# Optimization experiments

Measured on AMD Instinct MI355X. Metric: run time of the kernel, lower is better.

The kernel has to match this reference:

```python
import jax, jax.numpy as jnp
import numpy as np
from jax import lax

POOL_SIZE = 7
MERGE_INTERVAL = 1
NUM_FRAMES = 16_777_216  # 2**24, indices exact in float32
MAX_BEATS = NUM_FRAMES // 8  # fixed upper bound on number of merged-peak sections


def setup_inputs() -> dict:
    key = jax.random.key(0)
    logit = jax.random.normal(key, (1, NUM_FRAMES), dtype=jnp.float32)
    return {"logit": logit}


def reference(logit):
    # logit: (1, N)
    x = logit[0]  # (N,)
    N = x.shape[0]
    pad = POOL_SIZE // 2
    # max_pool1d, stride 1, same padding
    pooled = lax.reduce_window(x, -jnp.inf, lax.max,
                               window_dimensions=(POOL_SIZE,),
                               window_strides=(1,),
                               padding=((pad, pad),))
    # peak: position is a local max within the window AND value > 0
    peak = (x == pooled) & (x > 0)  # (N,) bool

    idx = jnp.arange(N, dtype=jnp.int32)
    # position of the most recent peak at or before each index (-1 if none)
    last_peak = lax.cummax(jnp.where(peak, idx, jnp.int32(-1)))
    # previous peak strictly before each index
    prev_peak = jnp.concatenate([jnp.full((1,), -1, jnp.int32), last_peak[:-1]])
    gap = idx - prev_peak
    # a peak starts a new section if gap to previous peak > merge_interval (first peak always new)
    is_new = peak & ((gap > MERGE_INTERVAL) | (prev_peak < 0))
    # section id per position (valid only at peaks); sections are contiguous 0..S-1
    section = jnp.cumsum(is_new.astype(jnp.int32)) - 1
    # route non-peaks to an overflow bucket
    seg_ids = jnp.where(peak, section, jnp.int32(MAX_BEATS))

    peak_f = peak.astype(jnp.float32)
    sum_peaks = jax.ops.segment_sum(idx.astype(jnp.float32) * peak_f, seg_ids,
                                    num_segments=MAX_BEATS + 1,
                                    indices_are_sorted=True)[:MAX_BEATS]
    count_peaks = jax.ops.segment_sum(peak_f, seg_ids,
                                      num_segments=MAX_BEATS + 1,
                                      indices_are_sorted=True)[:MAX_BEATS]
    # averaged beat positions; unused sections padded with -1 (torch returns a
    # dynamically-sized (1, num_sections) tensor; here first num_sections entries match)
    beats = jnp.where(count_peaks > 0,
                      sum_peaks / jnp.maximum(count_peaks, 1.0),
                      jnp.float32(-1.0))
    return beats[None, :]  # (1, MAX_BEATS)
```

## Files before the change

kernel.cpp:

```cpp
#include <hip/hip_runtime.h>
#include <cstdint>
#include <math.h>

#define N_FRAMES 16777216
#define MAX_BEATS (N_FRAMES / 8)
#define CHUNK 4096
#define NTHREADS 256
#define NBLOCKS (N_FRAMES / CHUNK)
#define TOTAL_MASKS ((size_t)NBLOCKS * 64)

typedef unsigned long long u64;
typedef unsigned int u32;

__device__ __forceinline__ bool peak_at_global(const float* __restrict__ x, int j) {
  if (j < 0 || j >= N_FRAMES) return false;
  const float c = x[j];
  if (!(c > 0.0f)) return false;
  float m = -INFINITY;
#pragma unroll
  for (int d = -3; d <= 3; ++d) {
    if (d == 0) continue;
    const int k = j + d;
    if (k >= 0 && k < N_FRAMES) m = fmaxf(m, x[k]);
  }
  return c >= m;
}

__global__ __launch_bounds__(NTHREADS) void k_count(const float* __restrict__ x,
                                                    int* __restrict__ blockCounts,
                                                    u64* __restrict__ masks) {
  __shared__ u32 m16[NTHREADS];
  __shared__ u32 s_pm1;
  const int b = blockIdx.x;
  const int g0 = b * CHUNK;
  const int t = threadIdx.x;
  const int gbase = g0 + t * 16;

  float v[24];
  if (gbase - 4 >= 0 && gbase + 20 <= N_FRAMES) {
    const float4* p = reinterpret_cast<const float4*>(x + gbase - 4);
#pragma unroll
    for (int k = 0; k < 6; ++k) {
      const float4 f = p[k];
      v[4 * k + 0] = f.x; v[4 * k + 1] = f.y; v[4 * k + 2] = f.z; v[4 * k + 3] = f.w;
    }
  } else {
#pragma unroll
    for (int k = 0; k < 24; ++k) {
      const int gi = gbase - 4 + k;
      v[k] = (gi >= 0 && gi < N_FRAMES) ? x[gi] : -INFINITY;
    }
  }

  u32 pm = 0;
#pragma unroll
  for (int e = 0; e < 16; ++e) {
    const float c = v[e + 4];
    float m = fmaxf(fmaxf(v[e + 1], v[e + 2]), fmaxf(v[e + 3], v[e + 5]));
    m = fmaxf(m, fmaxf(v[e + 6], v[e + 7]));
    pm |= (c > 0.0f && c >= m) ? (1u << e) : 0u;
  }
  m16[t] = pm;
  if (t == 0) {
    const float c = v[3];
    float m = fmaxf(fmaxf(v[0], v[1]), fmaxf(v[2], v[4]));
    m = fmaxf(m, fmaxf(v[5], v[6]));
    s_pm1 = (c > 0.0f && c >= m) ? 1u : 0u;
  }
  __syncthreads();

  if (t < 64) {
    const u64 m = (u64)m16[4 * t] | ((u64)m16[4 * t + 1] << 16) |
                  ((u64)m16[4 * t + 2] << 32) | ((u64)m16[4 * t + 3] << 48);
    masks[((size_t)b << 6) + t] = m;
    const u64 carry = (t == 0) ? (u64)s_pm1 : (u64)((m16[4 * t - 1] >> 15) & 1u);
    int cnt = __popcll(m & ~((m << 1) | carry));
#pragma unroll
    for (int off = 32; off; off >>= 1) cnt += __shfl_down(cnt, off, 64);
    if (t == 0) blockCounts[b] = cnt;
  }
}

__global__ __launch_bounds__(NTHREADS) void k_scan(const int* __restrict__ counts,
                                                   int* __restrict__ offsets) {
  __shared__ int wtot[4];
  const int t = threadIdx.x;
  const int w = t >> 6, lane = t & 63;
  int local[16];
  int s = 0;
#pragma unroll
  for (int e = 0; e < 16; ++e) { local[e] = counts[t * 16 + e]; s += local[e]; }
  int incl = s;
#pragma unroll
  for (int off = 1; off < 64; off <<= 1) {
    const int vv = __shfl_up(incl, off, 64);
    if (lane >= off) incl += vv;
  }
  if (lane == 63) wtot[w] = incl;
  __syncthreads();
  int wadd = 0;
  for (int ww = 0; ww < w; ++ww) wadd += wtot[ww];
  int excl = wadd + incl - s;
#pragma unroll
  for (int e = 0; e < 16; ++e) { offsets[t * 16 + e] = excl; excl += local[e]; }
  if (t == NTHREADS - 1) offsets[NBLOCKS] = excl;
}

__global__ __launch_bounds__(NTHREADS) void k_emit(const u64* __restrict__ masks,
                                                   const int* __restrict__ offsets,
                                                   float* __restrict__ out) {
  const int w = threadIdx.x >> 6, lane = threadIdx.x & 63;
  const int b = blockIdx.x * 4 + w;
  const size_t mi = ((size_t)b << 6) + lane;
  const u64 m = masks[mi];
  const u32 myb63 = (u32)(m >> 63);
  u32 prevb = __shfl_up(myb63, 1, 64);
  if (lane == 0) prevb = (b == 0) ? 0u : (u32)(masks[mi - 1] >> 63);
  u64 sm = m & ~((m << 1) | (u64)prevb);
  const int cnt = __popcll(sm);

  int incl = cnt;
#pragma unroll
  for (int off = 1; off < 64; off <<= 1) {
    const int vv = __shfl_up(incl, off, 64);
    if (lane >= off) incl += vv;
  }
  int sid = offsets[b] + incl - cnt;

  const int gbase = b * CHUNK + lane * 64;
  while (sm) {
    const int s = __builtin_ctzll(sm);
    sm &= sm - 1;
    const int i0 = gbase + s;
    const u64 above = m >> s;
    const int len = (~above == 0ull) ? (64 - s) : __builtin_ctzll(~above);
    int end = i0 + len - 1;
    if (s + len == 64) {
      size_t idx = mi + 1;
      while (idx < TOTAL_MASKS) {
        const u64 mm = masks[idx];
        if (~mm == 0ull) { end += 64; ++idx; }
        else { end += __builtin_ctzll(~mm); break; }
      }
    }
    if (sid < MAX_BEATS)
      out[sid] = (float)(((double)i0 + (double)end) * 0.5);
    ++sid;
  }

  const int total = offsets[NBLOCKS];
  const int lo = blockIdx.x * (MAX_BEATS / (NBLOCKS / 4));
  const int hi = lo + (MAX_BEATS / (NBLOCKS / 4));
  for (int i = max(lo, total) + (int)threadIdx.x; i < hi; i += NTHREADS)
    out[i] = -1.0f;
}

extern "C" void kernel_launch(void* const* d_in, const int* in_sizes, int n_in,
                              void* d_out, int out_size, void* d_ws, size_t ws_size,
                              hipStream_t stream) {
  const float* x = (const float*)d_in[0];
  float* out = (float*)d_out;

  u64* masks = (u64*)d_ws;
  int* counts = (int*)(masks + TOTAL_MASKS);
  int* offsets = counts + NBLOCKS;

  k_count<<<NBLOCKS, NTHREADS, 0, stream>>>(x, counts, masks);
  k_scan<<<1, NTHREADS, 0, stream>>>(counts, offsets);
  k_emit<<<NBLOCKS / 4, NTHREADS, 0, stream>>>(masks, offsets, out);
}
```

Measured before the change: 30.41 us.

## Drop the separate scan kernel and fold the offset scan into the emit kernel

Removes the single-block scan launch. Each emit block now reduces all 8192 per-wave counts itself and derives its own prefix offsets. The count kernel moves to 32 elements per thread with wave-level halos exchanged through shuffles instead of shared memory and block syncs, plus separable 3-wide max partials. Masks become 32-bit words. This saves one launch and its serialization, at the cost of every emit block redundantly reading 32 KB of counts.

```diff
diff --git a/kernel.cpp b/kernel.cpp
--- a/kernel.cpp
+++ b/kernel.cpp
@@ -4,143 +4,144 @@
 
 #define N_FRAMES 16777216
 #define MAX_BEATS (N_FRAMES / 8)
-#define CHUNK 4096
 #define NTHREADS 256
-#define NBLOCKS (N_FRAMES / CHUNK)
-#define TOTAL_MASKS ((size_t)NBLOCKS * 64)
+#define EPT 32
+#define EPB (NTHREADS * EPT)
+#define NBLOCKS (N_FRAMES / EPB)
+#define WCHUNK 2048
+#define NWCHUNK (N_FRAMES / WCHUNK)
+#define NMASK32 (N_FRAMES / 32)
 
-typedef unsigned long long u64;
 typedef unsigned int u32;
 
-__device__ __forceinline__ bool peak_at_global(const float* __restrict__ x, int j) {
-  if (j < 0 || j >= N_FRAMES) return false;
-  const float c = x[j];
-  if (!(c > 0.0f)) return false;
-  float m = -INFINITY;
+__global__ __launch_bounds__(NTHREADS) void k_count(const float* __restrict__ x,
+                                                    int* __restrict__ counts,
+                                                    u32* __restrict__ masks) {
+  const int t = threadIdx.x;
+  const int lane = t & 63;
+  const int wv = t >> 6;
+  const int q = blockIdx.x * 4 + wv;
+  const int gbase = q * WCHUNK + lane * EPT;
+
+  float v[40];
+  const float4* p = reinterpret_cast<const float4*>(x + gbase);
 #pragma unroll
-  for (int d = -3; d <= 3; ++d) {
-    if (d == 0) continue;
-    const int k = j + d;
-    if (k >= 0 && k < N_FRAMES) m = fmaxf(m, x[k]);
+  for (int k = 0; k < 8; ++k) {
+    const float4 f = p[k];
+    v[4 + 4 * k] = f.x; v[5 + 4 * k] = f.y; v[6 + 4 * k] = f.z; v[7 + 4 * k] = f.w;
   }
-  return c >= m;
-}
-
-__global__ __launch_bounds__(NTHREADS) void k_count(const float* __restrict__ x,
-                                                    int* __restrict__ blockCounts,
-                                                    u64* __restrict__ masks) {
-  __shared__ u32 m16[NTHREADS];
-  __shared__ u32 s_pm1;
-  const int b = blockIdx.x;
-  const int g0 = b * CHUNK;
-  const int t = threadIdx.x;
-  const int gbase = g0 + t * 16;
-
-  float v[24];
-  if (gbase - 4 >= 0 && gbase + 20 <= N_FRAMES) {
-    const float4* p = reinterpret_cast<const float4*>(x + gbase - 4);
 #pragma unroll
-    for (int k = 0; k < 6; ++k) {
-      const float4 f = p[k];
-      v[4 * k + 0] = f.x; v[4 * k + 1] = f.y; v[4 * k + 2] = f.z; v[4 * k + 3] = f.w;
+  for (int j = 0; j < 4; ++j) v[j] = __shfl_up(v[32 + j], 1, 64);
+#pragma unroll
+  for (int j = 0; j < 4; ++j) v[36 + j] = __shfl_down(v[4 + j], 1, 64);
+  if (lane == 0) {
+    if (gbase >= 4) {
+      const float4 f = *reinterpret_cast<const float4*>(x + gbase - 4);
+      v[0] = f.x; v[1] = f.y; v[2] = f.z; v[3] = f.w;
+    } else {
+      v[0] = v[1] = v[2] = v[3] = -INFINITY;
     }
-  } else {
-#pragma unroll
-    for (int k = 0; k < 24; ++k) {
-      const int gi = gbase - 4 + k;
-      v[k] = (gi >= 0 && gi < N_FRAMES) ? x[gi] : -INFINITY;
+  }
+  if (lane == 63) {
+    if (gbase + 36 <= N_FRAMES) {
+      const float4 f = *reinterpret_cast<const float4*>(x + gbase + 32);
+      v[36] = f.x; v[37] = f.y; v[38] = f.z; v[39] = f.w;
+    } else {
+      v[36] = v[37] = v[38] = v[39] = -INFINITY;
     }
   }
 
+  float Lt[37];
+#pragma unroll
+  for (int i = 0; i < 37; ++i) Lt[i] = fmaxf(fmaxf(v[i], v[i + 1]), v[i + 2]);
+
   u32 pm = 0;
 #pragma unroll
-  for (int e = 0; e < 16; ++e) {
+  for (int e = 0; e < 32; ++e) {
     const float c = v[e + 4];
-    float m = fmaxf(fmaxf(v[e + 1], v[e + 2]), fmaxf(v[e + 3], v[e + 5]));
-    m = fmaxf(m, fmaxf(v[e + 6], v[e + 7]));
-    pm |= (c > 0.0f && c >= m) ? (1u << e) : 0u;
+    const float m = fmaxf(Lt[e + 1], Lt[e + 5]);
+    if (c > 0.0f && c >= m) pm |= (1u << e);
   }
-  m16[t] = pm;
-  if (t == 0) {
+  masks[q * 64 + lane] = pm;
+
+  u32 prevbit = __shfl_up(pm, 1, 64) >> 31;
+  if (lane == 0) {
     const float c = v[3];
-    float m = fmaxf(fmaxf(v[0], v[1]), fmaxf(v[2], v[4]));
-    m = fmaxf(m, fmaxf(v[5], v[6]));
-    s_pm1 = (c > 0.0f && c >= m) ? 1u : 0u;
+    const float m = fmaxf(Lt[0], Lt[4]);
+    prevbit = (c > 0.0f && c >= m) ? 1u : 0u;
   }
-  __syncthreads();
-
-  if (t < 64) {
-    const u64 m = (u64)m16[4 * t] | ((u64)m16[4 * t + 1] << 16) |
-                  ((u64)m16[4 * t + 2] << 32) | ((u64)m16[4 * t + 3] << 48);
-    masks[((size_t)b << 6) + t] = m;
-    const u64 carry = (t == 0) ? (u64)s_pm1 : (u64)((m16[4 * t - 1] >> 15) & 1u);
-    int cnt = __popcll(m & ~((m << 1) | carry));
+  const u32 sm = pm & ~((pm << 1) | prevbit);
+  int cnt = __popc(sm);
 #pragma unroll
-    for (int off = 32; off; off >>= 1) cnt += __shfl_down(cnt, off, 64);
-    if (t == 0) blockCounts[b] = cnt;
-  }
+  for (int off = 32; off; off >>= 1) cnt += __shfl_down(cnt, off, 64);
+  if (lane == 0) counts[q] = cnt;
 }
 
-__global__ __launch_bounds__(NTHREADS) void k_scan(const int* __restrict__ counts,
-                                                   int* __restrict__ offsets) {
-  __shared__ int wtot[4];
+__global__ __launch_bounds__(NTHREADS) void k_emit(const u32* __restrict__ masks,
+                                                   const int* __restrict__ counts,
+                                                   float* __restrict__ out) {
+  __shared__ int s_wtot[4];
+  __shared__ int s_excl0[NTHREADS];
+  __shared__ int s_off[4];
+  __shared__ int s_total;
   const int t = threadIdx.x;
-  const int w = t >> 6, lane = t & 63;
-  int local[16];
+  const int lane = t & 63;
+  const int wv = t >> 6;
+
   int s = 0;
 #pragma unroll
-  for (int e = 0; e < 16; ++e) { local[e] = counts[t * 16 + e]; s += local[e]; }
+  for (int e = 0; e < 32; ++e) s += counts[t * 32 + e];
   int incl = s;
 #pragma unroll
   for (int off = 1; off < 64; off <<= 1) {
     const int vv = __shfl_up(incl, off, 64);
     if (lane >= off) incl += vv;
   }
-  if (lane == 63) wtot[w] = incl;
+  s_excl0[t] = incl - s;
+  if (lane == 63) s_wtot[wv] = incl;
   __syncthreads();
-  int wadd = 0;
-  for (int ww = 0; ww < w; ++ww) wadd += wtot[ww];
-  int excl = wadd + incl - s;
-#pragma unroll
-  for (int e = 0; e < 16; ++e) { offsets[t * 16 + e] = excl; excl += local[e]; }
-  if (t == NTHREADS - 1) offsets[NBLOCKS] = excl;
-}
+  if (t == 0) s_total = s_wtot[0] + s_wtot[1] + s_wtot[2] + s_wtot[3];
+  const int base = blockIdx.x * 4;
+  if (t < 4) {
+    const int target = base + t;
+    const int j = target >> 5, r = target & 31;
+    int wb = 0;
+    for (int ww = 0; ww < (j >> 6); ++ww) wb += s_wtot[ww];
+    int pfx = wb + s_excl0[j];
+    for (int e = 0; e < r; ++e) pfx += counts[j * 32 + e];
+    s_off[t] = pfx;
+  }
+  __syncthreads();
 
-__global__ __launch_bounds__(NTHREADS) void k_emit(const u64* __restrict__ masks,
-                                                   const int* __restrict__ offsets,
-                                                   float* __restrict__ out) {
-  const int w = threadIdx.x >> 6, lane = threadIdx.x & 63;
-  const int b = blockIdx.x * 4 + w;
-  const size_t mi = ((size_t)b << 6) + lane;
-  const u64 m = masks[mi];
-  const u32 myb63 = (u32)(m >> 63);
-  u32 prevb = __shfl_up(myb63, 1, 64);
-  if (lane == 0) prevb = (b == 0) ? 0u : (u32)(masks[mi - 1] >> 63);
-  u64 sm = m & ~((m << 1) | (u64)prevb);
-  const int cnt = __popcll(sm);
+  const int q = base + wv;
+  const u32 m = masks[q * 64 + lane];
+  u32 prevbit = __shfl_up(m, 1, 64) >> 31;
+  if (lane == 0) prevbit = (q == 0) ? 0u : (masks[q * 64 - 1] >> 31);
+  u32 sm = m & ~((m << 1) | prevbit);
+  const int cnt = __popc(sm);
 
-  int incl = cnt;
+  int incl2 = cnt;
 #pragma unroll
   for (int off = 1; off < 64; off <<= 1) {
-    const int vv = __shfl_up(incl, off, 64);
-    if (lane >= off) incl += vv;
+    const int vv = __shfl_up(incl2, off, 64);
+    if (lane >= off) incl2 += vv;
   }
-  int sid = offsets[b] + incl - cnt;
+  int sid = s_off[wv] + incl2 - cnt;
 
-  const int gbase = b * CHUNK + lane * 64;
+  const int gbase = q * WCHUNK + lane * 32;
   while (sm) {
-    const int s = __builtin_ctzll(sm);
+    const int sb = __builtin_ctz(sm);
     sm &= sm - 1;
-    const int i0 = gbase + s;
-    const u64 above = m >> s;
-    const int len = (~above == 0ull) ? (64 - s) : __builtin_ctzll(~above);
+    const int i0 = gbase + sb;
+    const u32 above = m >> sb;
+    const int len = (~above == 0u) ? (32 - sb) : __builtin_ctz(~above);
     int end = i0 + len - 1;
-    if (s + len == 64) {
-      size_t idx = mi + 1;
-      while (idx < TOTAL_MASKS) {
-        const u64 mm = masks[idx];
-        if (~mm == 0ull) { end += 64; ++idx; }
-        else { end += __builtin_ctzll(~mm); break; }
+    if (sb + len == 32) {
+      int idx = q * 64 + lane + 1;
+      while (idx < NMASK32) {
+        const u32 mm = masks[idx];
+        if (~mm == 0u) { end += 32; ++idx; }
+        else { end += __builtin_ctz(~mm); break; }
       }
     }
     if (sid < MAX_BEATS)
@@ -148,10 +149,9 @@
     ++sid;
   }
 
-  const int total = offsets[NBLOCKS];
-  const int lo = blockIdx.x * (MAX_BEATS / (NBLOCKS / 4));
-  const int hi = lo + (MAX_BEATS / (NBLOCKS / 4));
-  for (int i = max(lo, total) + (int)threadIdx.x; i < hi; i += NTHREADS)
+  const int lo = blockIdx.x * (MAX_BEATS / NBLOCKS);
+  const int hi = lo + (MAX_BEATS / NBLOCKS);
+  for (int i = max(lo, s_total) + t; i < hi; i += NTHREADS)
     out[i] = -1.0f;
 }
 
@@ -161,11 +161,9 @@
   const float* x = (const float*)d_in[0];
   float* out = (float*)d_out;
 
-  u64* masks = (u64*)d_ws;
-  int* counts = (int*)(masks + TOTAL_MASKS);
-  int* offsets = counts + NBLOCKS;
+  u32* masks = (u32*)d_ws;
+  int* counts = (int*)(masks + NMASK32);
 
   k_count<<<NBLOCKS, NTHREADS, 0, stream>>>(x, counts, masks);
-  k_scan<<<1, NTHREADS, 0, stream>>>(counts, offsets);
-  k_emit<<<NBLOCKS / 4, NTHREADS, 0, stream>>>(masks, offsets, out);
+  k_emit<<<NBLOCKS, NTHREADS, 0, stream>>>(masks, counts, out);
 }
```

New measurement: 32.78 us. 1.08x slower.

## Fuse block-count scan into emit kernel and share window max computation

Applied to the files above, without the earlier changes.

Removes the single-block scan kernel: each emit block now redundantly scans all 4096 chunk counts itself to find its own offsets and the total, which saves one launch and its serial dependency. The 7-wide window max is rebuilt from shared 3-wide partial maxima, cutting the number of fmax operations. Emission is skipped for waves whose base offset already exceeds MAX_BEATS. In exchange, every emit block re-reads the whole counts array.

```diff
diff --git a/kernel.cpp b/kernel.cpp
--- a/kernel.cpp
+++ b/kernel.cpp
@@ -6,28 +6,19 @@
 #define MAX_BEATS (N_FRAMES / 8)
 #define CHUNK 4096
 #define NTHREADS 256
-#define NBLOCKS (N_FRAMES / CHUNK)
-#define TOTAL_MASKS ((size_t)NBLOCKS * 64)
+#define NCHUNK (N_FRAMES / CHUNK)
+#define NBLK (NCHUNK / 4)
+#define TOTAL_MASKS ((size_t)NCHUNK * 64)
 
 typedef unsigned long long u64;
 typedef unsigned int u32;
 
-__device__ __forceinline__ bool peak_at_global(const float* __restrict__ x, int j) {
-  if (j < 0 || j >= N_FRAMES) return false;
-  const float c = x[j];
-  if (!(c > 0.0f)) return false;
-  float m = -INFINITY;
-#pragma unroll
-  for (int d = -3; d <= 3; ++d) {
-    if (d == 0) continue;
-    const int k = j + d;
-    if (k >= 0 && k < N_FRAMES) m = fmaxf(m, x[k]);
-  }
-  return c >= m;
+__device__ __forceinline__ float max3f(float a, float b, float c) {
+  return fmaxf(fmaxf(a, b), c);
 }
 
 __global__ __launch_bounds__(NTHREADS) void k_count(const float* __restrict__ x,
-                                                    int* __restrict__ blockCounts,
+                                                    int* __restrict__ counts,
                                                     u64* __restrict__ masks) {
   __shared__ u32 m16[NTHREADS];
   __shared__ u32 s_pm1;
@@ -52,19 +43,21 @@
     }
   }
 
+  float Lt[21];
+#pragma unroll
+  for (int i = 0; i < 21; ++i) Lt[i] = max3f(v[i], v[i + 1], v[i + 2]);
+
   u32 pm = 0;
 #pragma unroll
   for (int e = 0; e < 16; ++e) {
     const float c = v[e + 4];
-    float m = fmaxf(fmaxf(v[e + 1], v[e + 2]), fmaxf(v[e + 3], v[e + 5]));
-    m = fmaxf(m, fmaxf(v[e + 6], v[e + 7]));
-    pm |= (c > 0.0f && c >= m) ? (1u << e) : 0u;
+    const float m = fmaxf(Lt[e + 1], Lt[e + 5]);
+    if (c > 0.0f && c >= m) pm |= (1u << e);
   }
   m16[t] = pm;
   if (t == 0) {
     const float c = v[3];
-    float m = fmaxf(fmaxf(v[0], v[1]), fmaxf(v[2], v[4]));
-    m = fmaxf(m, fmaxf(v[5], v[6]));
+    const float m = fmaxf(Lt[0], Lt[4]);
     s_pm1 = (c > 0.0f && c >= m) ? 1u : 0u;
   }
   __syncthreads();
@@ -77,40 +70,45 @@
     int cnt = __popcll(m & ~((m << 1) | carry));
 #pragma unroll
     for (int off = 32; off; off >>= 1) cnt += __shfl_down(cnt, off, 64);
-    if (t == 0) blockCounts[b] = cnt;
+    if (t == 0) counts[b] = cnt;
   }
 }
 
-__global__ __launch_bounds__(NTHREADS) void k_scan(const int* __restrict__ counts,
-                                                   int* __restrict__ offsets) {
-  __shared__ int wtot[4];
-  const int t = threadIdx.x;
-  const int w = t >> 6, lane = t & 63;
-  int local[16];
+__global__ __launch_bounds__(NTHREADS) void k_emit(const u64* __restrict__ masks,
+                                                   const int* __restrict__ counts,
+                                                   float* __restrict__ out) {
+  __shared__ int s_wtot[4];
+  __shared__ int s_texcl[NTHREADS];
+  __shared__ int s_off[4];
+  __shared__ int s_total;
+  const int t = threadIdx.x, lane = t & 63, wv = t >> 6;
+
   int s = 0;
+  const int cb = t * 16;
 #pragma unroll
-  for (int e = 0; e < 16; ++e) { local[e] = counts[t * 16 + e]; s += local[e]; }
+  for (int e = 0; e < 16; ++e) s += counts[cb + e];
   int incl = s;
 #pragma unroll
   for (int off = 1; off < 64; off <<= 1) {
     const int vv = __shfl_up(incl, off, 64);
     if (lane >= off) incl += vv;
   }
-  if (lane == 63) wtot[w] = incl;
+  s_texcl[t] = incl - s;
+  if (lane == 63) s_wtot[wv] = incl;
   __syncthreads();
-  int wadd = 0;
-  for (int ww = 0; ww < w; ++ww) wadd += wtot[ww];
-  int excl = wadd + incl - s;
-#pragma unroll
-  for (int e = 0; e < 16; ++e) { offsets[t * 16 + e] = excl; excl += local[e]; }
-  if (t == NTHREADS - 1) offsets[NBLOCKS] = excl;
-}
+  if (t == 0) s_total = s_wtot[0] + s_wtot[1] + s_wtot[2] + s_wtot[3];
+  if (t < 4) {
+    const int target = blockIdx.x * 4 + t;
+    const int j = target >> 4, r = target & 15;
+    int wb = 0;
+    for (int ww = 0; ww < (j >> 6); ++ww) wb += s_wtot[ww];
+    int pfx = wb + s_texcl[j];
+    for (int e = 0; e < r; ++e) pfx += counts[j * 16 + e];
+    s_off[t] = pfx;
+  }
+  __syncthreads();
 
-__global__ __launch_bounds__(NTHREADS) void k_emit(const u64* __restrict__ masks,
-                                                   const int* __restrict__ offsets,
-                                                   float* __restrict__ out) {
-  const int w = threadIdx.x >> 6, lane = threadIdx.x & 63;
-  const int b = blockIdx.x * 4 + w;
+  const int b = blockIdx.x * 4 + wv;
   const size_t mi = ((size_t)b << 6) + lane;
   const u64 m = masks[mi];
   const u32 myb63 = (u32)(m >> 63);
@@ -119,39 +117,40 @@
   u64 sm = m & ~((m << 1) | (u64)prevb);
   const int cnt = __popcll(sm);
 
-  int incl = cnt;
+  int incl2 = cnt;
 #pragma unroll
   for (int off = 1; off < 64; off <<= 1) {
-    const int vv = __shfl_up(incl, off, 64);
-    if (lane >= off) incl += vv;
+    const int vv = __shfl_up(incl2, off, 64);
+    if (lane >= off) incl2 += vv;
   }
-  int sid = offsets[b] + incl - cnt;
+  int sid = s_off[wv] + incl2 - cnt;
 
-  const int gbase = b * CHUNK + lane * 64;
-  while (sm) {
-    const int s = __builtin_ctzll(sm);
-    sm &= sm - 1;
-    const int i0 = gbase + s;
-    const u64 above = m >> s;
-    const int len = (~above == 0ull) ? (64 - s) : __builtin_ctzll(~above);
-    int end = i0 + len - 1;
-    if (s + len == 64) {
-      size_t idx = mi + 1;
-      while (idx < TOTAL_MASKS) {
-        const u64 mm = masks[idx];
-        if (~mm == 0ull) { end += 64; ++idx; }
-        else { end += __builtin_ctzll(~mm); break; }
+  if (s_off[wv] < MAX_BEATS) {
+    const int gbase = b * CHUNK + lane * 64;
+    while (sm) {
+      const int sb = __builtin_ctzll(sm);
+      sm &= sm - 1;
+      const int i0 = gbase + sb;
+      const u64 above = m >> sb;
+      const int len = (~above == 0ull) ? (64 - sb) : __builtin_ctzll(~above);
+      int end = i0 + len - 1;
+      if (sb + len == 64) {
+        size_t idx = mi + 1;
+        while (idx < TOTAL_MASKS) {
+          const u64 mm = masks[idx];
+          if (~mm == 0ull) { end += 64; ++idx; }
+          else { end += __builtin_ctzll(~mm); break; }
+        }
       }
+      if (sid < MAX_BEATS)
+        out[sid] = (float)(((double)i0 + (double)end) * 0.5);
+      ++sid;
     }
-    if (sid < MAX_BEATS)
-      out[sid] = (float)(((double)i0 + (double)end) * 0.5);
-    ++sid;
   }
 
-  const int total = offsets[NBLOCKS];
-  const int lo = blockIdx.x * (MAX_BEATS / (NBLOCKS / 4));
-  const int hi = lo + (MAX_BEATS / (NBLOCKS / 4));
-  for (int i = max(lo, total) + (int)threadIdx.x; i < hi; i += NTHREADS)
+  const int lo = blockIdx.x * (MAX_BEATS / NBLK);
+  const int hi = lo + (MAX_BEATS / NBLK);
+  for (int i = max(lo, s_total) + t; i < hi; i += NTHREADS)
     out[i] = -1.0f;
 }
 
@@ -163,9 +162,7 @@
 
   u64* masks = (u64*)d_ws;
   int* counts = (int*)(masks + TOTAL_MASKS);
-  int* offsets = counts + NBLOCKS;
 
-  k_count<<<NBLOCKS, NTHREADS, 0, stream>>>(x, counts, masks);
-  k_scan<<<1, NTHREADS, 0, stream>>>(counts, offsets);
-  k_emit<<<NBLOCKS / 4, NTHREADS, 0, stream>>>(masks, offsets, out);
+  k_count<<<NCHUNK, NTHREADS, 0, stream>>>(x, counts, masks);
+  k_emit<<<NBLK, NTHREADS, 0, stream>>>(masks, counts, out);
 }
```

New measurement: 28.43 us. 1.07x faster.
